# Optimization experiments

Hardware: AMD Instinct MI355X
Metric: run time of the kernel (lower is better)

The kernel has to match this reference:

```python
import jax, jax.numpy as jnp
import numpy as np

N = 20000          # nodes
E = 320000         # edges (before self-loops)
H, C = 8, 32       # heads, hidden_size
ND, ED = 6, 11     # node_dim, edge_dim (hard-coded in module)
HC = H * C
DIFF_SCALE = 100.0
SLOPE = 0.2        # GATv2 leaky_relu negative_slope


def _glorot(k, shape):
    fan_in, fan_out = shape[0], shape[-1]
    lim = float(np.sqrt(6.0 / (fan_in + fan_out)))
    return jax.random.uniform(k, shape, jnp.float32, -lim, lim)


def setup_inputs() -> dict:
    key = jax.random.key(0)
    ks = jax.random.split(key, 16)
    d = {}
    d["x"] = jax.random.normal(ks[0], (N, ND), jnp.float32)
    d["edge_index"] = jax.random.randint(ks[1], (2, E), 0, N)
    d["edge_attr"] = jax.random.normal(ks[2], (E, ED), jnp.float32)
    # layer 0 (node_dim -> H*C, with edge features)
    d["Wl0"] = _glorot(ks[3], (ND, HC)); d["bl0"] = jnp.zeros((HC,), jnp.float32)
    d["Wr0"] = _glorot(ks[4], (ND, HC)); d["br0"] = jnp.zeros((HC,), jnp.float32)
    d["We0"] = _glorot(ks[5], (ED, HC))
    d["att0"] = _glorot(ks[6], (H, C))
    d["bias0"] = jnp.zeros((HC,), jnp.float32)
    # layer 1 (H*C -> H*C, no edge features)
    d["Wl1"] = _glorot(ks[7], (HC, HC)); d["bl1"] = jnp.zeros((HC,), jnp.float32)
    d["Wr1"] = _glorot(ks[8], (HC, HC)); d["br1"] = jnp.zeros((HC,), jnp.float32)
    d["att1"] = _glorot(ks[9], (H, C))
    d["bias1"] = jnp.zeros((HC,), jnp.float32)
    return d


def _gatv2(x, src, tgt, Wl, bl, Wr, br, att, bias, e=None, We=None):
    n = x.shape[0]
    xl = (x @ Wl + bl).reshape(n, H, C)   # source transform (messages)
    xr = (x @ Wr + br).reshape(n, H, C)   # target transform
    m = xl[src] + xr[tgt]                 # [E', H, C]
    if e is not None:
        m = m + (e @ We).reshape(-1, H, C)
    s = jax.nn.leaky_relu(m, SLOPE)
    logits = jnp.einsum('ehc,hc->eh', s, att)            # [E', H]
    # segment softmax over incoming edges of each target node
    mx = jax.ops.segment_max(logits, tgt, num_segments=n)
    ex = jnp.exp(logits - mx[tgt])
    den = jax.ops.segment_sum(ex, tgt, num_segments=n)
    alpha = ex / den[tgt]                                 # [E', H]
    out = jax.ops.segment_sum(alpha[:, :, None] * xl[src], tgt, num_segments=n)
    return out.reshape(n, HC) + bias


def reference(x, edge_index, edge_attr, Wl0, bl0, Wr0, br0, We0, att0, bias0,
              Wl1, bl1, Wr1, br1, att1, bias1):
    # preprocessing from GraphEmbedder.forward
    x = jnp.where((x[:, 2] == 1)[:, None] & (jnp.arange(ND) == 1)[None, :],
                  ((x[:, 1] - x[:, 0]) / DIFF_SCALE)[:, None], x)
    edge_attr = jnp.where((edge_attr[:, -2] == 1)[:, None] & (jnp.arange(ED) == 1)[None, :],
                          ((edge_attr[:, 1] - edge_attr[:, 0]) / DIFF_SCALE)[:, None], edge_attr)
    # add self-loops (PyG GATv2Conv default, fill_value='mean' for edge_attr)
    loop = jnp.arange(N)
    src = jnp.concatenate([edge_index[0], loop])
    tgt = jnp.concatenate([edge_index[1], loop])
    ea = jnp.concatenate([edge_attr, jnp.broadcast_to(edge_attr.mean(0), (N, ED))])
    h = _gatv2(x, src, tgt, Wl0, bl0, Wr0, br0, att0, bias0, e=ea, We=We0)
    h = jax.nn.elu(h)
    h = _gatv2(h, src, tgt, Wl1, bl1, Wr1, br1, att1, bias1)
    return h
```

## Files before the change

### kernel.cpp

```cpp
#include <hip/hip_runtime.h>
#include <cstddef>

#define N_H 8
#define N_C 32
#define N_HC 256
#define SLOPE 0.2f

typedef __attribute__((ext_vector_type(8))) short short8v;
typedef __attribute__((ext_vector_type(4))) float f32x4;

__device__ __forceinline__ short f2bf(float f) {
    unsigned u = __float_as_uint(f);
    unsigned r = (u + 0x7FFFu + ((u >> 16) & 1u)) >> 16;
    return (short)r;
}
__device__ __forceinline__ float bf2f(short s) {
    return __uint_as_float(((unsigned)(unsigned short)s) << 16);
}

__global__ __launch_bounds__(256) void ea_colsum_kernel(const float* __restrict__ ea,
                                                        float* __restrict__ sums, int E) {
    float loc[11];
#pragma unroll
    for (int j = 0; j < 11; ++j) loc[j] = 0.f;
    for (int i = blockIdx.x * blockDim.x + threadIdx.x; i < E; i += gridDim.x * blockDim.x) {
        float r[11];
#pragma unroll
        for (int j = 0; j < 11; ++j) r[j] = ea[i * 11 + j];
        if (r[9] == 1.0f) r[1] = (r[1] - r[0]) * 0.01f;
#pragma unroll
        for (int j = 0; j < 11; ++j) loc[j] += r[j];
    }
    __shared__ float sbuf[256];
#pragma unroll
    for (int j = 0; j < 11; ++j) {
        sbuf[threadIdx.x] = loc[j];
        __syncthreads();
        for (int s = 128; s > 0; s >>= 1) {
            if (threadIdx.x < s) sbuf[threadIdx.x] += sbuf[threadIdx.x + s];
            __syncthreads();
        }
        if (threadIdx.x == 0) atomicAdd(&sums[j], sbuf[0]);
        __syncthreads();
    }
}

__global__ void mean_div_kernel(const float* __restrict__ sums, float* __restrict__ mean, int E) {
    int t = threadIdx.x;
    if (t < 11) mean[t] = sums[t] / (float)E;
}

__global__ __launch_bounds__(256) void deg_hist_kernel(const int* __restrict__ ei,
                                                       int* __restrict__ deg, int E, int Etot) {
    int e = blockIdx.x * blockDim.x + threadIdx.x;
    if (e >= Etot) return;
    int t = (e < E) ? ei[E + e] : e - E;
    atomicAdd(&deg[t], 1);
}

__global__ __launch_bounds__(1024) void scan_kernel(const int* __restrict__ deg,
                                                    int* __restrict__ offs,
                                                    int* __restrict__ cursor, int Nn) {
    const int T = 1024;
    int tid = threadIdx.x;
    int chunk = (Nn + T - 1) / T;
    int b = tid * chunk;
    int s = 0;
    for (int k = 0; k < chunk; ++k) {
        int i = b + k;
        if (i < Nn) s += deg[i];
    }
    __shared__ int sm[T];
    sm[tid] = s;
    __syncthreads();
    for (int d = 1; d < T; d <<= 1) {
        int v = (tid >= d) ? sm[tid - d] : 0;
        __syncthreads();
        sm[tid] += v;
        __syncthreads();
    }
    int pref = (tid > 0) ? sm[tid - 1] : 0;
    for (int k = 0; k < chunk; ++k) {
        int i = b + k;
        if (i < Nn) {
            offs[i] = pref;
            cursor[i] = pref;
            pref += deg[i];
        }
    }
    if (tid == T - 1) offs[Nn] = sm[T - 1];
}

__global__ __launch_bounds__(256) void scatter_kernel(const int* __restrict__ ei,
                                                      const float* __restrict__ ea,
                                                      const float* __restrict__ mean_ea,
                                                      int* __restrict__ cursor,
                                                      int* __restrict__ esrc,
                                                      float* __restrict__ ea_csr, int E,
                                                      int Etot) {
    int e = blockIdx.x * blockDim.x + threadIdx.x;
    if (e >= Etot) return;
    int s, t;
    if (e < E) { s = ei[e]; t = ei[E + e]; }
    else       { s = t = e - E; }
    int pos = atomicAdd(&cursor[t], 1);
    esrc[pos] = s;
    float r[11];
    if (e < E) {
#pragma unroll
        for (int j = 0; j < 11; ++j) r[j] = ea[(size_t)e * 11 + j];
        if (r[9] == 1.0f) r[1] = (r[1] - r[0]) * 0.01f;
    } else {
#pragma unroll
        for (int j = 0; j < 11; ++j) r[j] = mean_ea[j];
    }
    float* dst = ea_csr + (size_t)pos * 12;
#pragma unroll
    for (int j = 0; j < 11; ++j) dst[j] = r[j];
}

template <int K, int R>
__global__ __launch_bounds__(256) void node_mm_kernel(const float* __restrict__ X,
                                                      const float* __restrict__ Wl,
                                                      const float* __restrict__ bl,
                                                      const float* __restrict__ Wr,
                                                      const float* __restrict__ br,
                                                      float* __restrict__ xl,
                                                      float* __restrict__ xr, int Nn) {
    __shared__ float xs[R][K];
    int row0 = blockIdx.x * R;
    int tid = threadIdx.x;
    for (int i = tid; i < R * K; i += blockDim.x) {
        int r = i / K, k = i - r * K;
        int gr = row0 + r;
        float v = 0.f;
        if (gr < Nn) {
            v = X[(size_t)gr * K + k];
            if (k == 1) {
                float x0 = X[(size_t)gr * K + 0];
                float x2 = X[(size_t)gr * K + 2];
                if (x2 == 1.0f) v = (v - x0) * 0.01f;
            }
        }
        xs[r][k] = v;
    }
    __syncthreads();
    int c = tid;
    float accl[R], accr[R];
#pragma unroll
    for (int r = 0; r < R; ++r) { accl[r] = bl[c]; accr[r] = br[c]; }
#pragma unroll
    for (int k = 0; k < K; ++k) {
        float wl = Wl[k * N_HC + c], wr = Wr[k * N_HC + c];
#pragma unroll
        for (int r = 0; r < R; ++r) {
            accl[r] = fmaf(xs[r][k], wl, accl[r]);
            accr[r] = fmaf(xs[r][k], wr, accr[r]);
        }
    }
#pragma unroll
    for (int r = 0; r < R; ++r) {
        int gr = row0 + r;
        if (gr < Nn) {
            xl[(size_t)gr * N_HC + c] = accl[r];
            xr[(size_t)gr * N_HC + c] = accr[r];
        }
    }
}

__global__ __launch_bounds__(256) void convert_w_kernel(const float* __restrict__ Wl,
                                                        const float* __restrict__ Wr,
                                                        short* __restrict__ Bfhi,
                                                        short* __restrict__ Bflo) {
    int n = blockIdx.x;
    int k = threadIdx.x;
    float v = (n < 256) ? Wl[(size_t)k * 256 + n] : Wr[(size_t)k * 256 + (n - 256)];
    short hi = f2bf(v);
    short lo = f2bf(v - bf2f(hi));
    int cg = n >> 6, ni = (n >> 4) & 3, lm = n & 15;
    int k0 = k >> 5, lg = (k >> 3) & 3, e = k & 7;
    int lane = lg * 16 + lm;
    size_t idx = ((((size_t)cg * 8 + k0) * 4 + ni) * 64 + lane) * 8 + e;
    Bfhi[idx] = hi;
    Bflo[idx] = lo;
}

__global__ __launch_bounds__(256) void gemm_mfma_kernel(
    const short* __restrict__ Ahi, const short* __restrict__ Alo,
    const short* __restrict__ Bfhi, const short* __restrict__ Bflo,
    const float* __restrict__ bl, const float* __restrict__ br, float* __restrict__ xl,
    float* __restrict__ xr, int Nn) {
    const int wid = threadIdx.x >> 6, lane = threadIdx.x & 63;
    const int lm = lane & 15, lg = lane >> 4;
    const int r0 = blockIdx.x * 16;
    const int half = blockIdx.y;
    const int cg = half * 4 + wid;
    const int kg = lg * 8;

    f32x4 acc0 = {0.f, 0.f, 0.f, 0.f}, acc1 = acc0, acc2 = acc0, acc3 = acc0;

    const int rA = r0 + lm;
    const bool va = rA < Nn;
    const short* pah = Ahi + (size_t)rA * 256 + kg;
    const short* pal = Alo + (size_t)rA * 256 + kg;
    const short8v zz = (short8v)0;

#pragma unroll 2
    for (int ks = 0; ks < 8; ++ks) {
        const int k0 = ks * 32;
        short8v ah = va ? *(const short8v*)(pah + k0) : zz;
        short8v al = va ? *(const short8v*)(pal + k0) : zz;
        const size_t fb = (((size_t)cg * 8 + ks) * 4) * 512 + (size_t)lane * 8;
        const short8v bh0 = *(const short8v*)(Bfhi + fb + 0 * 512);
        const short8v bl0 = *(const short8v*)(Bflo + fb + 0 * 512);
        const short8v bh1 = *(const short8v*)(Bfhi + fb + 1 * 512);
        const short8v bl1 = *(const short8v*)(Bflo + fb + 1 * 512);
        const short8v bh2 = *(const short8v*)(Bfhi + fb + 2 * 512);
        const short8v bl2 = *(const short8v*)(Bflo + fb + 2 * 512);
        const short8v bh3 = *(const short8v*)(Bfhi + fb + 3 * 512);
        const short8v bl3 = *(const short8v*)(Bflo + fb + 3 * 512);
        acc0 = __builtin_amdgcn_mfma_f32_16x16x32_bf16(ah, bh0, acc0, 0, 0, 0);
        acc0 = __builtin_amdgcn_mfma_f32_16x16x32_bf16(al, bh0, acc0, 0, 0, 0);
        acc0 = __builtin_amdgcn_mfma_f32_16x16x32_bf16(ah, bl0, acc0, 0, 0, 0);
        acc1 = __builtin_amdgcn_mfma_f32_16x16x32_bf16(ah, bh1, acc1, 0, 0, 0);
        acc1 = __builtin_amdgcn_mfma_f32_16x16x32_bf16(al, bh1, acc1, 0, 0, 0);
        acc1 = __builtin_amdgcn_mfma_f32_16x16x32_bf16(ah, bl1, acc1, 0, 0, 0);
        acc2 = __builtin_amdgcn_mfma_f32_16x16x32_bf16(ah, bh2, acc2, 0, 0, 0);
        acc2 = __builtin_amdgcn_mfma_f32_16x16x32_bf16(al, bh2, acc2, 0, 0, 0);
        acc2 = __builtin_amdgcn_mfma_f32_16x16x32_bf16(ah, bl2, acc2, 0, 0, 0);
        acc3 = __builtin_amdgcn_mfma_f32_16x16x32_bf16(ah, bh3, acc3, 0, 0, 0);
        acc3 = __builtin_amdgcn_mfma_f32_16x16x32_bf16(al, bh3, acc3, 0, 0, 0);
        acc3 = __builtin_amdgcn_mfma_f32_16x16x32_bf16(ah, bl3, acc3, 0, 0, 0);
    }

    const float* __restrict__ bias = half ? br : bl;
    float* __restrict__ dst = half ? xr : xl;
    const int clbase = wid * 64 + lm;
#pragma unroll
    for (int ni = 0; ni < 4; ++ni) {
        int col = clbase + ni * 16;
        float bv = bias[col];
        f32x4 a = (ni == 0) ? acc0 : (ni == 1) ? acc1 : (ni == 2) ? acc2 : acc3;
        int rb = r0 + lg * 4;
#pragma unroll
        for (int e = 0; e < 4; ++e) {
            int row = rb + e;
            if (row < Nn) dst[(size_t)row * N_HC + col] = a[e] + bv;
        }
    }
}

__global__ __launch_bounds__(256) void gemm256_kernel(const float* __restrict__ X,
                                                      const float* __restrict__ Wl,
                                                      const float* __restrict__ bl,
                                                      const float* __restrict__ Wr,
                                                      const float* __restrict__ br,
                                                      float* __restrict__ xl,
                                                      float* __restrict__ xr, int Nn) {
    __shared__ float As[32][128];
    __shared__ float Bs[32][128];

    const int by = blockIdx.y;
    const float* __restrict__ W = (by < 2) ? Wl : Wr;
    const float* __restrict__ bias = (by < 2) ? bl : br;
    float* __restrict__ dst = (by < 2) ? xl : xr;
    const int cb = (by & 1) * 128;
    const int row0 = blockIdx.x * 128;
    const int tid = threadIdx.x;
    const int tx = tid & 15, ty = tid >> 4;
    const int tx4 = tx * 4, ty4 = ty * 4;

    const int arow = tid & 127;
    const int akh = (tid >> 7) * 16;
    const int bk0 = tid >> 5;
    const int bc4 = (tid & 31) * 4;

    float acc[8][8];
#pragma unroll
    for (int i = 0; i < 8; ++i)
#pragma unroll
        for (int j = 0; j < 8; ++j) acc[i][j] = 0.f;

    const int garow = row0 + arow;
    const bool aval = garow < Nn;
    const float* __restrict__ asrc = X + (size_t)garow * 256 + akh;

    for (int s = 0; s < 256; s += 32) {
        float4 av[4];
#pragma unroll
        for (int q = 0; q < 4; ++q)
            av[q] = aval ? *(const float4*)(asrc + s + q * 4) : float4{0.f, 0.f, 0.f, 0.f};
#pragma unroll
        for (int q = 0; q < 4; ++q) {
            As[akh + q * 4 + 0][arow] = av[q].x;
            As[akh + q * 4 + 1][arow] = av[q].y;
            As[akh + q * 4 + 2][arow] = av[q].z;
            As[akh + q * 4 + 3][arow] = av[q].w;
        }
#pragma unroll
        for (int q = 0; q < 4; ++q) {
            int kr = bk0 + q * 8;
            *(float4*)&Bs[kr][bc4] = *(const float4*)(W + (size_t)(s + kr) * 256 + cb + bc4);
        }
        __syncthreads();
#pragma unroll 8
        for (int k = 0; k < 32; ++k) {
            const float4 a0 = *(const float4*)&As[k][ty4];
            const float4 a1 = *(const float4*)&As[k][64 + ty4];
            const float4 b0 = *(const float4*)&Bs[k][tx4];
            const float4 b1 = *(const float4*)&Bs[k][64 + tx4];
            const float ar[8] = {a0.x, a0.y, a0.z, a0.w, a1.x, a1.y, a1.z, a1.w};
            const float brr[8] = {b0.x, b0.y, b0.z, b0.w, b1.x, b1.y, b1.z, b1.w};
#pragma unroll
            for (int i = 0; i < 8; ++i)
#pragma unroll
                for (int j = 0; j < 8; ++j) acc[i][j] = fmaf(ar[i], brr[j], acc[i][j]);
        }
        __syncthreads();
    }

    const float4 bv0 = *(const float4*)(bias + cb + tx4);
    const float4 bv1 = *(const float4*)(bias + cb + 64 + tx4);
#pragma unroll
    for (int i = 0; i < 8; ++i) {
        int r = row0 + ((i < 4) ? (ty4 + i) : (64 + ty4 + i - 4));
        if (r < Nn) {
            float4 u0 = {acc[i][0] + bv0.x, acc[i][1] + bv0.y, acc[i][2] + bv0.z,
                         acc[i][3] + bv0.w};
            float4 u1 = {acc[i][4] + bv1.x, acc[i][5] + bv1.y, acc[i][6] + bv1.z,
                         acc[i][7] + bv1.w};
            *(float4*)(dst + (size_t)r * N_HC + cb + tx4) = u0;
            *(float4*)(dst + (size_t)r * N_HC + cb + 64 + tx4) = u1;
        }
    }
}

__device__ __forceinline__ void online_update(float logit, const float4& xlv, float& m,
                                              float& den, float4& acc) {
    float mn = fmaxf(m, logit);
    float s = __expf(m - mn);
    float w = __expf(logit - mn);
    den = den * s + w;
    acc.x = fmaf(w, xlv.x, acc.x * s);
    acc.y = fmaf(w, xlv.y, acc.y * s);
    acc.z = fmaf(w, xlv.z, acc.z * s);
    acc.w = fmaf(w, xlv.w, acc.w * s);
    m = mn;
}

template <bool L0>
__device__ __forceinline__ float edge_logit(const float4& xlv, const float4& xrv,
                                            const float4* Wreg, const float* __restrict__ eap,
                                            const float4& av) {
    float m0 = xlv.x + xrv.x, m1 = xlv.y + xrv.y, m2 = xlv.z + xrv.z, m3 = xlv.w + xrv.w;
    if (L0) {
#pragma unroll
        for (int j = 0; j < 11; ++j) {
            float aj = eap[j];
            m0 = fmaf(aj, Wreg[j].x, m0);
            m1 = fmaf(aj, Wreg[j].y, m1);
            m2 = fmaf(aj, Wreg[j].z, m2);
            m3 = fmaf(aj, Wreg[j].w, m3);
        }
    }
    m0 = m0 > 0.f ? m0 : SLOPE * m0;
    m1 = m1 > 0.f ? m1 : SLOPE * m1;
    m2 = m2 > 0.f ? m2 : SLOPE * m2;
    m3 = m3 > 0.f ? m3 : SLOPE * m3;
    float p = m0 * av.x + m1 * av.y + m2 * av.z + m3 * av.w;
    p += __shfl_xor(p, 1);
    p += __shfl_xor(p, 2);
    p += __shfl_xor(p, 4);
    return p;
}

template <bool L0>
__global__ __launch_bounds__(256) void node_gather_kernel(
    const int* __restrict__ offs, const int* __restrict__ esrc,
    const float* __restrict__ ea_csr, const float* __restrict__ We,
    const float* __restrict__ att, const float* __restrict__ xl, const float* __restrict__ xr,
    const float* __restrict__ bias, float* __restrict__ out, short* __restrict__ oAhi,
    short* __restrict__ oAlo, int Nn) {
    int wid = threadIdx.x >> 6;
    int lane = threadIdx.x & 63;
    int node = blockIdx.x * 4 + wid;
    if (node >= Nn) return;
    int c4 = lane * 4;

    float4 Wreg[11];
    if (L0) {
#pragma unroll
        for (int j = 0; j < 11; ++j) Wreg[j] = *(const float4*)(We + j * N_HC + c4);
    }
    const float4 xrv = *(const float4*)(xr + (size_t)node * N_HC + c4);
    const float4 av = *(const float4*)(att + c4);

    int beg = offs[node], end = offs[node + 1];

    float mA = -INFINITY, dA = 0.f;
    float mB = -INFINITY, dB = 0.f;
    float mC = -INFINITY, dC = 0.f;
    float mD = -INFINITY, dD = 0.f;
    float4 aA = {0.f, 0.f, 0.f, 0.f}, aB = aA, aC = aA, aD = aA;

    int p = beg;
    for (; p + 3 < end; p += 4) {
        int pu = __builtin_amdgcn_readfirstlane(p);
        int s0 = esrc[pu + 0];
        int s1 = esrc[pu + 1];
        int s2 = esrc[pu + 2];
        int s3 = esrc[pu + 3];
        const float4 x0 = *(const float4*)(xl + (size_t)s0 * N_HC + c4);
        const float4 x1 = *(const float4*)(xl + (size_t)s1 * N_HC + c4);
        const float4 x2 = *(const float4*)(xl + (size_t)s2 * N_HC + c4);
        const float4 x3 = *(const float4*)(xl + (size_t)s3 * N_HC + c4);
        const float* e0 = L0 ? (ea_csr + (size_t)(pu + 0) * 12) : nullptr;
        const float* e1 = L0 ? (ea_csr + (size_t)(pu + 1) * 12) : nullptr;
        const float* e2 = L0 ? (ea_csr + (size_t)(pu + 2) * 12) : nullptr;
        const float* e3 = L0 ? (ea_csr + (size_t)(pu + 3) * 12) : nullptr;
        float lg0 = edge_logit<L0>(x0, xrv, Wreg, e0, av);
        float lg1 = edge_logit<L0>(x1, xrv, Wreg, e1, av);
        float lg2 = edge_logit<L0>(x2, xrv, Wreg, e2, av);
        float lg3 = edge_logit<L0>(x3, xrv, Wreg, e3, av);
        online_update(lg0, x0, mA, dA, aA);
        online_update(lg1, x1, mB, dB, aB);
        online_update(lg2, x2, mC, dC, aC);
        online_update(lg3, x3, mD, dD, aD);
    }
    for (; p < end; ++p) {
        int pu = __builtin_amdgcn_readfirstlane(p);
        int s0 = esrc[pu];
        const float4 x0 = *(const float4*)(xl + (size_t)s0 * N_HC + c4);
        const float* e0 = L0 ? (ea_csr + (size_t)pu * 12) : nullptr;
        float lg0 = edge_logit<L0>(x0, xrv, Wreg, e0, av);
        online_update(lg0, x0, mA, dA, aA);
    }

    float mm = fmaxf(fmaxf(mA, mB), fmaxf(mC, mD));
    float sA = __expf(mA - mm), sB = __expf(mB - mm);
    float sC = __expf(mC - mm), sD = __expf(mD - mm);
    float den = dA * sA + dB * sB + dC * sC + dD * sD;
    float4 acct;
    acct.x = aA.x * sA + aB.x * sB + aC.x * sC + aD.x * sD;
    acct.y = aA.y * sA + aB.y * sB + aC.y * sC + aD.y * sD;
    acct.z = aA.z * sA + aB.z * sB + aC.z * sC + aD.z * sD;
    acct.w = aA.w * sA + aB.w * sB + aC.w * sC + aD.w * sD;

    const float4 bv = *(const float4*)(bias + c4);
    float4 r;
    r.x = acct.x / den + bv.x;
    r.y = acct.y / den + bv.y;
    r.z = acct.z / den + bv.z;
    r.w = acct.w / den + bv.w;
    if (L0) {
        r.x = r.x > 0.f ? r.x : (__expf(r.x) - 1.f);
        r.y = r.y > 0.f ? r.y : (__expf(r.y) - 1.f);
        r.z = r.z > 0.f ? r.z : (__expf(r.z) - 1.f);
        r.w = r.w > 0.f ? r.w : (__expf(r.w) - 1.f);
    }
    if (oAhi) {
        short h0 = f2bf(r.x), h1 = f2bf(r.y), h2 = f2bf(r.z), h3 = f2bf(r.w);
        short4 hv = {h0, h1, h2, h3};
        short4 lv = {f2bf(r.x - bf2f(h0)), f2bf(r.y - bf2f(h1)), f2bf(r.z - bf2f(h2)),
                     f2bf(r.w - bf2f(h3))};
        *(short4*)(oAhi + (size_t)node * N_HC + c4) = hv;
        *(short4*)(oAlo + (size_t)node * N_HC + c4) = lv;
    } else {
        *(float4*)(out + (size_t)node * N_HC + c4) = r;
    }
}

extern "C" void kernel_launch(void* const* d_in, const int* in_sizes, int n_in, void* d_out,
                              int out_size, void* d_ws, size_t ws_size, hipStream_t stream) {
    const float* x = (const float*)d_in[0];
    const int* ei = (const int*)d_in[1];
    const float* ea = (const float*)d_in[2];
    const float* Wl0 = (const float*)d_in[3];
    const float* bl0 = (const float*)d_in[4];
    const float* Wr0 = (const float*)d_in[5];
    const float* br0 = (const float*)d_in[6];
    const float* We0 = (const float*)d_in[7];
    const float* att0 = (const float*)d_in[8];
    const float* bias0 = (const float*)d_in[9];
    const float* Wl1 = (const float*)d_in[10];
    const float* bl1 = (const float*)d_in[11];
    const float* Wr1 = (const float*)d_in[12];
    const float* br1 = (const float*)d_in[13];
    const float* att1 = (const float*)d_in[14];
    const float* bias1 = (const float*)d_in[15];
    float* out = (float*)d_out;

    const int Nn = in_sizes[0] / 6;
    const int E = in_sizes[1] / 2;
    const int Etot = E + Nn;

    auto align16 = [](size_t v) { return (v + 15) & ~(size_t)15; };
    float* ws = (float*)d_ws;
    size_t o = 0;
    float* xl = ws + o;     o = align16(o + (size_t)Nn * N_HC);
    float* xr = ws + o;     o = align16(o + (size_t)Nn * N_HC);
    float* h = ws + o;      o = align16(o + (size_t)Nn * N_HC);
    float* ea_csr = ws + o; o = align16(o + (size_t)Etot * 12);
    float* easum = ws + o;  o = align16(o + 16);
    float* mean = ws + o;   o = align16(o + 16);
    int* deg = (int*)(ws + o);    o = align16(o + (size_t)Nn);
    int* offs = (int*)(ws + o);   o = align16(o + (size_t)Nn + 1);
    int* cursor = (int*)(ws + o); o = align16(o + (size_t)Nn);
    int* esrc = (int*)(ws + o);   o = align16(o + (size_t)Etot);
    short* Bfhi = (short*)(ws + o); o = align16(o + 512 * 256 / 2);
    short* Bflo = (short*)(ws + o); o = align16(o + 512 * 256 / 2);
    const bool use_mfma = (o * sizeof(float) <= ws_size);

    hipMemsetAsync(easum, 0, 16 * sizeof(float), stream);
    hipMemsetAsync(deg, 0, (size_t)Nn * sizeof(int), stream);

    ea_colsum_kernel<<<256, 256, 0, stream>>>(ea, easum, E);
    mean_div_kernel<<<1, 32, 0, stream>>>(easum, mean, E);

    deg_hist_kernel<<<(Etot + 255) / 256, 256, 0, stream>>>(ei, deg, E, Etot);
    scan_kernel<<<1, 1024, 0, stream>>>(deg, offs, cursor, Nn);
    scatter_kernel<<<(Etot + 255) / 256, 256, 0, stream>>>(ei, ea, mean, cursor, esrc, ea_csr, E,
                                                           Etot);

    const int gblocks = (Nn + 3) / 4;

    short* Ahi = (short*)d_out;
    short* Alo = Ahi + (size_t)Nn * N_HC;

    node_mm_kernel<6, 8><<<(Nn + 7) / 8, 256, 0, stream>>>(x, Wl0, bl0, Wr0, br0, xl, xr, Nn);
    node_gather_kernel<true><<<gblocks, 256, 0, stream>>>(offs, esrc, ea_csr, We0, att0, xl, xr,
                                                          bias0, h, use_mfma ? Ahi : nullptr,
                                                          use_mfma ? Alo : nullptr, Nn);

    if (use_mfma) {
        convert_w_kernel<<<512, 256, 0, stream>>>(Wl1, Wr1, Bfhi, Bflo);
        dim3 mgrid((Nn + 15) / 16, 2);
        gemm_mfma_kernel<<<mgrid, 256, 0, stream>>>(Ahi, Alo, Bfhi, Bflo, bl1, br1, xl, xr, Nn);
    } else {
        dim3 ggrid((Nn + 127) / 128, 4);
        gemm256_kernel<<<ggrid, 256, 0, stream>>>(h, Wl1, bl1, Wr1, br1, xl, xr, Nn);
    }
    node_gather_kernel<false><<<gblocks, 256, 0, stream>>>(offs, esrc, nullptr, nullptr, att1, xl,
                                                           xr, bias1, out, nullptr, nullptr, Nn);
}
```

Before: 296.0 us.

## Split each node's edge list across two wavefronts and merge softmax partials in LDS

The gather kernel now runs two wavefronts per target node, each handling half of the incoming edges. Each produces online-softmax partials (max, denominator, accumulator), and these are merged through shared memory after a block barrier. The goal is more memory-level parallelism and more waves in flight for the latency-bound gather of xl rows, with an average degree of about 17. The cost is a __syncthreads, LDS traffic, duplicated per-wave setup such as loading We and xr, and guards for empty halves through expdiff.

```diff
diff --git a/kernel.cpp b/kernel.cpp
--- a/kernel.cpp
+++ b/kernel.cpp
@@ -16,6 +16,9 @@
 }
 __device__ __forceinline__ float bf2f(short s) {
     return __uint_as_float(((unsigned)(unsigned short)s) << 16);
+}
+__device__ __forceinline__ float expdiff(float a, float b) {
+    return (a == -INFINITY) ? 0.f : __expf(a - b);
 }
 
 __global__ __launch_bounds__(256) void ea_colsum_kernel(const float* __restrict__ ea,
@@ -375,27 +378,33 @@
 }
 
 template <bool L0>
-__global__ __launch_bounds__(256) void node_gather_kernel(
+__global__ __launch_bounds__(512) void node_gather_kernel(
     const int* __restrict__ offs, const int* __restrict__ esrc,
     const float* __restrict__ ea_csr, const float* __restrict__ We,
     const float* __restrict__ att, const float* __restrict__ xl, const float* __restrict__ xr,
     const float* __restrict__ bias, float* __restrict__ out, short* __restrict__ oAhi,
     short* __restrict__ oAlo, int Nn) {
-    int wid = threadIdx.x >> 6;
-    int lane = threadIdx.x & 63;
-    int node = blockIdx.x * 4 + wid;
-    if (node >= Nn) return;
-    int c4 = lane * 4;
+    const int w = threadIdx.x >> 6;
+    const int lane = threadIdx.x & 63;
+    const int half = w >> 2;
+    const int node = blockIdx.x * 4 + (w & 3);
+    const bool valid = node < Nn;
+    const int nc = valid ? node : 0;
+    const int c4 = lane * 4;
 
     float4 Wreg[11];
     if (L0) {
 #pragma unroll
         for (int j = 0; j < 11; ++j) Wreg[j] = *(const float4*)(We + j * N_HC + c4);
     }
-    const float4 xrv = *(const float4*)(xr + (size_t)node * N_HC + c4);
     const float4 av = *(const float4*)(att + c4);
-
-    int beg = offs[node], end = offs[node + 1];
+    const float4 xrv = *(const float4*)(xr + (size_t)nc * N_HC + c4);
+
+    int beg = offs[nc], end = offs[nc + 1];
+    if (!valid) end = beg;
+    const int mid = beg + ((end - beg) >> 1);
+    int p = half ? mid : beg;
+    const int pe = half ? end : mid;
 
     float mA = -INFINITY, dA = 0.f;
     float mB = -INFINITY, dB = 0.f;
@@ -403,8 +412,7 @@
     float mD = -INFINITY, dD = 0.f;
     float4 aA = {0.f, 0.f, 0.f, 0.f}, aB = aA, aC = aA, aD = aA;
 
-    int p = beg;
-    for (; p + 3 < end; p += 4) {
+    for (; p + 3 < pe; p += 4) {
         int pu = __builtin_amdgcn_readfirstlane(p);
         int s0 = esrc[pu + 0];
         int s1 = esrc[pu + 1];
@@ -427,7 +435,7 @@
         online_update(lg2, x2, mC, dC, aC);
         online_update(lg3, x3, mD, dD, aD);
     }
-    for (; p < end; ++p) {
+    for (; p < pe; ++p) {
         int pu = __builtin_amdgcn_readfirstlane(p);
         int s0 = esrc[pu];
         const float4 x0 = *(const float4*)(xl + (size_t)s0 * N_HC + c4);
@@ -437,36 +445,59 @@
     }
 
     float mm = fmaxf(fmaxf(mA, mB), fmaxf(mC, mD));
-    float sA = __expf(mA - mm), sB = __expf(mB - mm);
-    float sC = __expf(mC - mm), sD = __expf(mD - mm);
-    float den = dA * sA + dB * sB + dC * sC + dD * sD;
-    float4 acct;
-    acct.x = aA.x * sA + aB.x * sB + aC.x * sC + aD.x * sD;
-    acct.y = aA.y * sA + aB.y * sB + aC.y * sC + aD.y * sD;
-    acct.z = aA.z * sA + aB.z * sB + aC.z * sC + aD.z * sD;
-    acct.w = aA.w * sA + aB.w * sB + aC.w * sC + aD.w * sD;
-
-    const float4 bv = *(const float4*)(bias + c4);
-    float4 r;
-    r.x = acct.x / den + bv.x;
-    r.y = acct.y / den + bv.y;
-    r.z = acct.z / den + bv.z;
-    r.w = acct.w / den + bv.w;
-    if (L0) {
-        r.x = r.x > 0.f ? r.x : (__expf(r.x) - 1.f);
-        r.y = r.y > 0.f ? r.y : (__expf(r.y) - 1.f);
-        r.z = r.z > 0.f ? r.z : (__expf(r.z) - 1.f);
-        r.w = r.w > 0.f ? r.w : (__expf(r.w) - 1.f);
-    }
-    if (oAhi) {
-        short h0 = f2bf(r.x), h1 = f2bf(r.y), h2 = f2bf(r.z), h3 = f2bf(r.w);
-        short4 hv = {h0, h1, h2, h3};
-        short4 lv = {f2bf(r.x - bf2f(h0)), f2bf(r.y - bf2f(h1)), f2bf(r.z - bf2f(h2)),
-                     f2bf(r.w - bf2f(h3))};
-        *(short4*)(oAhi + (size_t)node * N_HC + c4) = hv;
-        *(short4*)(oAlo + (size_t)node * N_HC + c4) = lv;
-    } else {
-        *(float4*)(out + (size_t)node * N_HC + c4) = r;
+    float sA = expdiff(mA, mm), sB = expdiff(mB, mm);
+    float sC = expdiff(mC, mm), sD = expdiff(mD, mm);
+    float den1 = dA * sA + dB * sB + dC * sC + dD * sD;
+    float4 a1;
+    a1.x = aA.x * sA + aB.x * sB + aC.x * sC + aD.x * sD;
+    a1.y = aA.y * sA + aB.y * sB + aC.y * sC + aD.y * sD;
+    a1.z = aA.z * sA + aB.z * sB + aC.z * sC + aD.z * sD;
+    a1.w = aA.w * sA + aB.w * sB + aC.w * sC + aD.w * sD;
+
+    __shared__ float smrg[8][64][6];
+    smrg[w][lane][0] = mm;
+    smrg[w][lane][1] = den1;
+    smrg[w][lane][2] = a1.x;
+    smrg[w][lane][3] = a1.y;
+    smrg[w][lane][4] = a1.z;
+    smrg[w][lane][5] = a1.w;
+    __syncthreads();
+    if (w < 4 && valid) {
+        float m2 = smrg[w + 4][lane][0];
+        float d2 = smrg[w + 4][lane][1];
+        float4 a2 = {smrg[w + 4][lane][2], smrg[w + 4][lane][3], smrg[w + 4][lane][4],
+                     smrg[w + 4][lane][5]};
+        float M = fmaxf(mm, m2);
+        float s1 = expdiff(mm, M), s2 = expdiff(m2, M);
+        float den = den1 * s1 + d2 * s2;
+        float4 acct;
+        acct.x = a1.x * s1 + a2.x * s2;
+        acct.y = a1.y * s1 + a2.y * s2;
+        acct.z = a1.z * s1 + a2.z * s2;
+        acct.w = a1.w * s1 + a2.w * s2;
+
+        const float4 bv = *(const float4*)(bias + c4);
+        float4 r;
+        r.x = acct.x / den + bv.x;
+        r.y = acct.y / den + bv.y;
+        r.z = acct.z / den + bv.z;
+        r.w = acct.w / den + bv.w;
+        if (L0) {
+            r.x = r.x > 0.f ? r.x : (__expf(r.x) - 1.f);
+            r.y = r.y > 0.f ? r.y : (__expf(r.y) - 1.f);
+            r.z = r.z > 0.f ? r.z : (__expf(r.z) - 1.f);
+            r.w = r.w > 0.f ? r.w : (__expf(r.w) - 1.f);
+        }
+        if (oAhi) {
+            short h0 = f2bf(r.x), h1 = f2bf(r.y), h2 = f2bf(r.z), h3 = f2bf(r.w);
+            short4 hv = {h0, h1, h2, h3};
+            short4 lv = {f2bf(r.x - bf2f(h0)), f2bf(r.y - bf2f(h1)), f2bf(r.z - bf2f(h2)),
+                         f2bf(r.w - bf2f(h3))};
+            *(short4*)(oAhi + (size_t)node * N_HC + c4) = hv;
+            *(short4*)(oAlo + (size_t)node * N_HC + c4) = lv;
+        } else {
+            *(float4*)(out + (size_t)node * N_HC + c4) = r;
+        }
     }
 }
 
@@ -528,7 +559,7 @@
     short* Alo = Ahi + (size_t)Nn * N_HC;
 
     node_mm_kernel<6, 8><<<(Nn + 7) / 8, 256, 0, stream>>>(x, Wl0, bl0, Wr0, br0, xl, xr, Nn);
-    node_gather_kernel<true><<<gblocks, 256, 0, stream>>>(offs, esrc, ea_csr, We0, att0, xl, xr,
+    node_gather_kernel<true><<<gblocks, 512, 0, stream>>>(offs, esrc, ea_csr, We0, att0, xl, xr,
                                                           bias0, h, use_mfma ? Ahi : nullptr,
                                                           use_mfma ? Alo : nullptr, Nn);
 
@@ -540,6 +571,6 @@
         dim3 ggrid((Nn + 127) / 128, 4);
         gemm256_kernel<<<ggrid, 256, 0, stream>>>(h, Wl1, bl1, Wr1, br1, xl, xr, Nn);
     }
-    node_gather_kernel<false><<<gblocks, 256, 0, stream>>>(offs, esrc, nullptr, nullptr, att1, xl,
+    node_gather_kernel<false><<<gblocks, 512, 0, stream>>>(offs, esrc, nullptr, nullptr, att1, xl,
                                                            xr, bias1, out, nullptr, nullptr, Nn);
 }
```

Measured after the change: 312.9 us. +5.7%, slower.
